# Optimization experiments

Measured on AMD Instinct MI355X. Metric: run time of the kernel, lower is better.

The kernel has to match this reference:

```python
import jax, jax.numpy as jnp
import numpy as np

N_NODES = 100000
N_EDGES = 1600000
D_FEAT = 128
NUM_UNITS = 128


def setup_inputs() -> dict:
    key = jax.random.key(0)
    k1, k2, k3, k4, k5 = jax.random.split(key, 5)
    H = jax.random.normal(k1, (N_NODES, D_FEAT), dtype=jnp.float32)
    edge_vals = jax.random.uniform(k2, (N_EDGES,), dtype=jnp.float32)
    W = jax.random.normal(k3, (D_FEAT, NUM_UNITS), dtype=jnp.float32) / np.sqrt(D_FEAT)
    b = jnp.zeros((NUM_UNITS,), dtype=jnp.float32)
    edge_src = jax.random.randint(k4, (N_EDGES,), 0, N_NODES, dtype=jnp.int32)
    edge_dst = jax.random.randint(k5, (N_EDGES,), 0, N_NODES, dtype=jnp.int32)
    return {"H": H, "edge_vals": edge_vals, "W": W, "b": b,
            "edge_src": edge_src, "edge_dst": edge_dst}


def reference(H, edge_vals, W, b, edge_src, edge_dst):
    # SpMM: AH[i] = sum_{e: src[e]==i} val[e] * H[dst[e]]
    gathered = edge_vals[:, None] * H[edge_dst]            # [E, F]
    AH = jax.ops.segment_sum(gathered, edge_src, num_segments=N_NODES)  # [N, F]
    # Dense projection + bias + relu (tf.layers.Dense with tf.nn.relu)
    return jax.nn.relu(AH @ W + b)
```

## Files before the change

kernel.cpp:

```cpp
#include <hip/hip_runtime.h>

#define N_NODES  100000
#define N_EDGES  1600000
#define D        128
#define CB       782
#define CCAP     3072
#define SUBCAP   768
#define OCAP     8192
#define FCHUNK   8192
#define FILL_BLOCKS ((N_EDGES + FCHUNK - 1) / FCHUNK)
#define NSG      3125

typedef __attribute__((ext_vector_type(8))) short bf16x8;
typedef __attribute__((ext_vector_type(4))) float f32x4;

__device__ __forceinline__ unsigned short f2bf(float x) {
    unsigned u = __float_as_uint(x);
    u += 0x7fffu + ((u >> 16) & 1u);
    return (unsigned short)(u >> 16);
}

__global__ __launch_bounds__(256) void init_kernel(
    const float* __restrict__ W, unsigned short* __restrict__ Wfrag,
    int* __restrict__ ccursor)
{
    int t = blockIdx.x * 256 + threadIdx.x;
    if (t <= CB) ccursor[t] = 0;
    int k = t >> 7, n = t & 127;
    int c = n >> 4, cc = n & 15, ks = k >> 5, g = (k >> 3) & 3, j = k & 7;
    int lane = g * 16 + cc;
    Wfrag[(size_t)(((c * 4 + ks) * 64) + lane) * 8 + j] = f2bf(W[t]);
}

__global__ __launch_bounds__(256) void fill_bucket(
    const int* __restrict__ src, const int* __restrict__ dst,
    const float* __restrict__ vals, int* __restrict__ ccursor,
    int2* __restrict__ sedge_raw, int4* __restrict__ oflow,
    int* __restrict__ oflow_cnt)
{
    __shared__ int lhist[CB];
    __shared__ int lbase[CB];
    const int t = threadIdx.x;
    for (int i = t; i < CB; i += 256) lhist[i] = 0;
    __syncthreads();
    const int e0 = blockIdx.x * FCHUNK;
    const int e1 = min(e0 + FCHUNK, N_EDGES);
    for (int e = e0 + t; e < e1; e += 256)
        atomicAdd(&lhist[src[e] >> 7], 1);
    __syncthreads();
    for (int i = t; i < CB; i += 256) {
        int c = lhist[i];
        lbase[i] = c ? atomicAdd(&ccursor[i], c) : 0;
        lhist[i] = 0;
    }
    __syncthreads();
    for (int e = e0 + t; e < e1; e += 256) {
        int s = src[e];
        int bkt = s >> 7;
        int pos = lbase[bkt] + atomicAdd(&lhist[bkt], 1);
        if (pos < CCAP) {
            int2 p;
            p.x = dst[e] | ((s & 127) << 17);
            p.y = __float_as_int(vals[e]);
            sedge_raw[(size_t)bkt * CCAP + pos] = p;
        } else {
            int oc = atomicAdd(oflow_cnt, 1);
            if (oc < OCAP) oflow[oc] = make_int4(s, dst[e], __float_as_int(vals[e]), 0);
        }
    }
}

__global__ __launch_bounds__(256) void gemm_mfma(
    const float* __restrict__ H, const unsigned short* __restrict__ Wfrag,
    unsigned short* __restrict__ HWb)
{
    const int wid  = threadIdx.x >> 6;
    const int lane = threadIdx.x & 63;
    const int row16 = blockIdx.x * 64 + wid * 16;
    const int g = lane >> 4;

    int arow = row16 + (lane & 15);
    if (arow >= N_NODES) arow = N_NODES - 1;

    f32x4 acc[8];
#pragma unroll
    for (int c = 0; c < 8; ++c) acc[c] = (f32x4){0.f, 0.f, 0.f, 0.f};

#pragma unroll
    for (int ks = 0; ks < 4; ++ks) {
        const float* ap = H + (size_t)arow * D + ks * 32 + g * 8;
        float4 a0 = *reinterpret_cast<const float4*>(ap);
        float4 a1 = *reinterpret_cast<const float4*>(ap + 4);
        bf16x8 af;
        af[0] = (short)f2bf(a0.x); af[1] = (short)f2bf(a0.y);
        af[2] = (short)f2bf(a0.z); af[3] = (short)f2bf(a0.w);
        af[4] = (short)f2bf(a1.x); af[5] = (short)f2bf(a1.y);
        af[6] = (short)f2bf(a1.z); af[7] = (short)f2bf(a1.w);
#pragma unroll
        for (int c = 0; c < 8; ++c) {
            bf16x8 bf = *reinterpret_cast<const bf16x8*>(
                Wfrag + (size_t)((c * 4 + ks) * 64 + lane) * 8);
            acc[c] = __builtin_amdgcn_mfma_f32_16x16x32_bf16(af, bf, acc[c], 0, 0, 0);
        }
    }

#pragma unroll
    for (int c = 0; c < 8; ++c) {
#pragma unroll
        for (int r = 0; r < 4; ++r) {
            int orow = row16 + g * 4 + r;
            if (orow < N_NODES)
                HWb[(size_t)orow * D + c * 16 + (lane & 15)] = f2bf(acc[c][r]);
        }
    }
}

__global__ __launch_bounds__(256) void sort_gather(
    const unsigned short* __restrict__ HWb, const int2* __restrict__ sedge_raw,
    const int* __restrict__ ccursor, const int4* __restrict__ oflow,
    const int* __restrict__ oflow_cnt, const float* __restrict__ bias,
    float* __restrict__ out)
{
    __shared__ int2 eLds[SUBCAP];
    __shared__ int h[32];
    __shared__ int ex[32];
    __shared__ int cur[32];
    const int cb  = blockIdx.x >> 2;
    const int sub = blockIdx.x & 3;
    const int t = threadIdx.x;
    const size_t base = (size_t)cb * CCAP;
    const int cnt = min(ccursor[cb], CCAP);

    if (t < 32) h[t] = 0;
    __syncthreads();

    int2 myE[12]; int myR[12];
#pragma unroll
    for (int q = 0; q < 12; ++q) {
        int j = t + q * 256;
        myR[q] = -1;
        if (j < cnt) {
            int2 e = sedge_raw[base + j];
            if (((e.x >> 22) & 3) == sub) {
                myE[q] = e;
                myR[q] = (e.x >> 17) & 31;
                atomicAdd(&h[myR[q]], 1);
            }
        }
    }
    __syncthreads();
    if (t < 32) {
        int v = h[t];
        int x = v;
        for (int off = 1; off < 32; off <<= 1) {
            int y = __shfl_up(x, off);
            if (t >= off) x += y;
        }
        ex[t] = x - v;
        cur[t] = 0;
    }
    __syncthreads();
#pragma unroll
    for (int q = 0; q < 12; ++q) {
        if (myR[q] >= 0) {
            int pos = ex[myR[q]] + atomicAdd(&cur[myR[q]], 1);
            if (pos < SUBCAP) {
                int2 e;
                e.x = myE[q].x & 0x1FFFF;
                e.y = myE[q].y;
                eLds[pos] = e;
            }
        }
    }
    __syncthreads();

    const int wid = t >> 6, lane = t & 63;
    const int ovc = *oflow_cnt;
    const float2 bv = *reinterpret_cast<const float2*>(bias + lane * 2);
    for (int ln = wid; ln < 32; ln += 4) {
        int node = cb * 128 + sub * 32 + ln;
        if (node >= N_NODES) break;
        int j0 = ex[ln], j1 = min(ex[ln] + h[ln], SUBCAP);
        float ax = 0.f, ay = 0.f, bx = 0.f, by = 0.f;
        float cx = 0.f, cy = 0.f, dx = 0.f, dy = 0.f;
        int j = j0;
        for (; j + 4 <= j1; j += 4) {
            int2 e0 = eLds[j],     e1 = eLds[j + 1];
            int2 e2 = eLds[j + 2], e3 = eLds[j + 3];
            unsigned u0 = *reinterpret_cast<const unsigned*>(HWb + (size_t)e0.x * D + lane * 2);
            unsigned u1 = *reinterpret_cast<const unsigned*>(HWb + (size_t)e1.x * D + lane * 2);
            unsigned u2 = *reinterpret_cast<const unsigned*>(HWb + (size_t)e2.x * D + lane * 2);
            unsigned u3 = *reinterpret_cast<const unsigned*>(HWb + (size_t)e3.x * D + lane * 2);
            float v0 = __int_as_float(e0.y), v1 = __int_as_float(e1.y);
            float v2 = __int_as_float(e2.y), v3 = __int_as_float(e3.y);
            ax += v0 * __uint_as_float(u0 << 16);
            ay += v0 * __uint_as_float(u0 & 0xffff0000u);
            bx += v1 * __uint_as_float(u1 << 16);
            by += v1 * __uint_as_float(u1 & 0xffff0000u);
            cx += v2 * __uint_as_float(u2 << 16);
            cy += v2 * __uint_as_float(u2 & 0xffff0000u);
            dx += v3 * __uint_as_float(u3 << 16);
            dy += v3 * __uint_as_float(u3 & 0xffff0000u);
        }
        for (; j < j1; ++j) {
            int2 e = eLds[j];
            unsigned u = *reinterpret_cast<const unsigned*>(HWb + (size_t)e.x * D + lane * 2);
            float v = __int_as_float(e.y);
            ax += v * __uint_as_float(u << 16);
            ay += v * __uint_as_float(u & 0xffff0000u);
        }
        for (int q = 0; q < ovc; ++q) {
            int4 e = oflow[q];
            if (e.x == node) {
                unsigned u = *reinterpret_cast<const unsigned*>(HWb + (size_t)e.y * D + lane * 2);
                float v = __int_as_float(e.z);
                ax += v * __uint_as_float(u << 16);
                ay += v * __uint_as_float(u & 0xffff0000u);
            }
        }
        float2 o;
        o.x = fmaxf((ax + bx) + (cx + dx) + bv.x, 0.f);
        o.y = fmaxf((ay + by) + (cy + dy) + bv.y, 0.f);
        *reinterpret_cast<float2*>(out + (size_t)node * D + lane * 2) = o;
    }
}

extern "C" void kernel_launch(void* const* d_in, const int* in_sizes, int n_in,
                              void* d_out, int out_size, void* d_ws, size_t ws_size,
                              hipStream_t stream) {
    const float* H    = (const float*)d_in[0];
    const float* vals = (const float*)d_in[1];
    const float* W    = (const float*)d_in[2];
    const float* b    = (const float*)d_in[3];
    const int*   src  = (const int*)d_in[4];
    const int*   dst  = (const int*)d_in[5];
    float* out = (float*)d_out;

    unsigned short* HWb   = (unsigned short*)d_ws;
    unsigned short* Wfrag = HWb + (size_t)N_NODES * D;
    int2* sedge_raw = (int2*)(Wfrag + 128 * 128);
    int*  ccursor   = (int*)(sedge_raw + (size_t)CB * CCAP);
    int*  oflow_cnt = ccursor + CB;
    int4* oflow     = (int4*)(oflow_cnt + 3);

    init_kernel<<<64, 256, 0, stream>>>(W, Wfrag, ccursor);
    fill_bucket<<<FILL_BLOCKS, 256, 0, stream>>>(src, dst, vals, ccursor,
                                                 sedge_raw, oflow, oflow_cnt);
    gemm_mfma<<<(N_NODES + 63) / 64, 256, 0, stream>>>(H, Wfrag, HWb);
    sort_gather<<<NSG, 256, 0, stream>>>(HWb, sedge_raw, ccursor, oflow,
                                         oflow_cnt, b, out);
}
```

Measured before the change: 134.3 us.

## Add split pass partitioning coarse buckets into per-subblock buckets before gather

Adds a split_bucket kernel that partitions each 128-node coarse bucket into four 32-node sub-buckets, spilling entries past the capacity to the overflow list. sort_gather then reads only its own sub-bucket (up to 3 entries per thread instead of 12) rather than scanning the whole coarse bucket and discarding three quarters of it. This removes 4x redundant reads of the coarse bucket data in the gather kernel. In exchange it adds an extra launch plus a full read and write of the edge array, and changes the workspace layout.

```diff
diff --git a/kernel.cpp b/kernel.cpp
--- a/kernel.cpp
+++ b/kernel.cpp
@@ -5,6 +5,7 @@
 #define D        128
 #define CB       782
 #define CCAP     3072
+#define NFB      (CB * 4)
 #define SUBCAP   768
 #define OCAP     8192
 #define FCHUNK   8192
@@ -70,6 +71,35 @@
     }
 }
 
+__global__ __launch_bounds__(256) void split_bucket(
+    const int2* __restrict__ sedge_raw, const int* __restrict__ ccursor,
+    int2* __restrict__ sedge, int* __restrict__ scursor,
+    int4* __restrict__ oflow, int* __restrict__ oflow_cnt)
+{
+    __shared__ int cur4[4];
+    const int cb = blockIdx.x;
+    const int t = threadIdx.x;
+    const int n = min(ccursor[cb], CCAP);
+    if (t < 4) cur4[t] = 0;
+    __syncthreads();
+    for (int j = t; j < n; j += 256) {
+        int2 e = sedge_raw[(size_t)cb * CCAP + j];
+        int g = (e.x >> 22) & 3;
+        int pos = atomicAdd(&cur4[g], 1);
+        if (pos < SUBCAP) {
+            sedge[((size_t)cb * 4 + g) * SUBCAP + pos] = e;
+        } else {
+            int oc = atomicAdd(oflow_cnt, 1);
+            if (oc < OCAP) {
+                int node = (cb << 7) | ((e.x >> 17) & 127);
+                oflow[oc] = make_int4(node, e.x & 0x1FFFF, e.y, 0);
+            }
+        }
+    }
+    __syncthreads();
+    if (t < 4) scursor[cb * 4 + t] = min(cur4[t], SUBCAP);
+}
+
 __global__ __launch_bounds__(256) void gemm_mfma(
     const float* __restrict__ H, const unsigned short* __restrict__ Wfrag,
     unsigned short* __restrict__ HWb)
@@ -116,8 +146,8 @@
 }
 
 __global__ __launch_bounds__(256) void sort_gather(
-    const unsigned short* __restrict__ HWb, const int2* __restrict__ sedge_raw,
-    const int* __restrict__ ccursor, const int4* __restrict__ oflow,
+    const unsigned short* __restrict__ HWb, const int2* __restrict__ sedge,
+    const int* __restrict__ scursor, const int4* __restrict__ oflow,
     const int* __restrict__ oflow_cnt, const float* __restrict__ bias,
     float* __restrict__ out)
 {
@@ -125,27 +155,23 @@
     __shared__ int h[32];
     __shared__ int ex[32];
     __shared__ int cur[32];
-    const int cb  = blockIdx.x >> 2;
-    const int sub = blockIdx.x & 3;
+    const int bkt = blockIdx.x;
     const int t = threadIdx.x;
-    const size_t base = (size_t)cb * CCAP;
-    const int cnt = min(ccursor[cb], CCAP);
+    const size_t base = (size_t)bkt * SUBCAP;
+    const int cnt = scursor[bkt];
 
     if (t < 32) h[t] = 0;
     __syncthreads();
 
-    int2 myE[12]; int myR[12];
-#pragma unroll
-    for (int q = 0; q < 12; ++q) {
+    int2 myE[3]; int myR[3];
+#pragma unroll
+    for (int q = 0; q < 3; ++q) {
         int j = t + q * 256;
         myR[q] = -1;
         if (j < cnt) {
-            int2 e = sedge_raw[base + j];
-            if (((e.x >> 22) & 3) == sub) {
-                myE[q] = e;
-                myR[q] = (e.x >> 17) & 31;
-                atomicAdd(&h[myR[q]], 1);
-            }
+            myE[q] = sedge[base + j];
+            myR[q] = (myE[q].x >> 17) & 31;
+            atomicAdd(&h[myR[q]], 1);
         }
     }
     __syncthreads();
@@ -161,15 +187,13 @@
     }
     __syncthreads();
 #pragma unroll
-    for (int q = 0; q < 12; ++q) {
+    for (int q = 0; q < 3; ++q) {
         if (myR[q] >= 0) {
             int pos = ex[myR[q]] + atomicAdd(&cur[myR[q]], 1);
-            if (pos < SUBCAP) {
-                int2 e;
-                e.x = myE[q].x & 0x1FFFF;
-                e.y = myE[q].y;
-                eLds[pos] = e;
-            }
+            int2 e;
+            e.x = myE[q].x & 0x1FFFF;
+            e.y = myE[q].y;
+            eLds[pos] = e;
         }
     }
     __syncthreads();
@@ -178,9 +202,8 @@
     const int ovc = *oflow_cnt;
     const float2 bv = *reinterpret_cast<const float2*>(bias + lane * 2);
     for (int ln = wid; ln < 32; ln += 4) {
-        int node = cb * 128 + sub * 32 + ln;
-        if (node >= N_NODES) break;
-        int j0 = ex[ln], j1 = min(ex[ln] + h[ln], SUBCAP);
+        int node = bkt * 32 + ln;
+        const int j0 = ex[ln], j1 = ex[ln] + h[ln];
         float ax = 0.f, ay = 0.f, bx = 0.f, by = 0.f;
         float cx = 0.f, cy = 0.f, dx = 0.f, dy = 0.f;
         int j = j0;
@@ -239,14 +262,18 @@
     unsigned short* HWb   = (unsigned short*)d_ws;
     unsigned short* Wfrag = HWb + (size_t)N_NODES * D;
     int2* sedge_raw = (int2*)(Wfrag + 128 * 128);
-    int*  ccursor   = (int*)(sedge_raw + (size_t)CB * CCAP);
+    int2* sedge     = sedge_raw + (size_t)CB * CCAP;
+    int*  ccursor   = (int*)(sedge + (size_t)NFB * SUBCAP);
     int*  oflow_cnt = ccursor + CB;
-    int4* oflow     = (int4*)(oflow_cnt + 3);
+    int*  scursor   = oflow_cnt + 1;
+    int4* oflow     = (int4*)(((uintptr_t)(scursor + NFB) + 15) & ~(uintptr_t)15);
 
     init_kernel<<<64, 256, 0, stream>>>(W, Wfrag, ccursor);
     fill_bucket<<<FILL_BLOCKS, 256, 0, stream>>>(src, dst, vals, ccursor,
                                                  sedge_raw, oflow, oflow_cnt);
+    split_bucket<<<CB, 256, 0, stream>>>(sedge_raw, ccursor, sedge, scursor,
+                                         oflow, oflow_cnt);
     gemm_mfma<<<(N_NODES + 63) / 64, 256, 0, stream>>>(H, Wfrag, HWb);
-    sort_gather<<<NSG, 256, 0, stream>>>(HWb, sedge_raw, ccursor, oflow,
+    sort_gather<<<NSG, 256, 0, stream>>>(HWb, sedge, scursor, oflow,
                                          oflow_cnt, b, out);
 }
```

Result: no change. 134.6 us (+0.2%).
